# Performance work log

Measured on AMD Instinct MI355X. Metric: run time of the kernel, lower is better.

Reference implementation:

```python
import jax, jax.numpy as jnp
import numpy as np

NUM_TIME_BLOCKS = 32  # P
B, L, D = 32, 4096, 256


def setup_inputs() -> dict:
    key = jax.random.key(0)
    k1, k2 = jax.random.split(key)
    x = jax.random.normal(k1, (B, L, D), dtype=jnp.float32)
    # normalized timestamps in [0, 1), matching linspace(0, 1.001, P+1) bin edges
    time_steps = jax.random.uniform(k2, (B, L), dtype=jnp.float32)
    return {"x": x, "time_steps": time_steps}


def reference(x, time_steps):
    # Bin edges identical to torch.linspace(0.0, 1.001, P+1)
    blocks = jnp.linspace(0.0, 1.001, NUM_TIME_BLOCKS + 1, dtype=jnp.float32)
    ls = blocks[:-1]  # (P,) left edges (inclusive)
    rs = blocks[1:]   # (P,) right edges (exclusive)
    ts = time_steps[..., None]                      # (B, L, 1)
    # one-hot bucket membership mask, (B, L, P); a token falls in exactly one bin
    mask = ((ts >= ls) & (ts < rs)).astype(x.dtype)
    # sum x over sequence positions within each time bucket -> (B, P, D)
    new_x = jnp.einsum('blp,bld->bpd', mask, x)
    return new_x, time_steps
```

## Files before the change

### kernel.cpp

```cpp
#include <hip/hip_runtime.h>


#define Bk 32
#define Lk 4096
#define Dk 256
#define Pk 32

__device__ __forceinline__ int bucket_of(float tv) {
    const double step = 1.001 / 32.0;
    int p = (int)(tv * (float)(32.0 / 1.001));
    p = p < 0 ? 0 : (p > 31 ? 31 : p);
    while (p > 0 && tv < (float)((double)p * step)) --p;
    while (p < 31 && tv >= (float)((double)(p + 1) * step)) ++p;
    return p;
}

__global__ __launch_bounds__(256) void tc_fused(
        const float* __restrict__ x,
        const float* __restrict__ ts,
        float* __restrict__ out,
        float* __restrict__ ts_out) {
    __shared__ int rows[Lk];
    __shared__ int nrows;
    __shared__ float red[4 * Dk];

    const int p = blockIdx.x;
    const int b = blockIdx.y;
    const int t = threadIdx.x;
    const int w = t >> 6;
    const int lane = t & 63;
    const int col4 = lane << 2;

    if (t == 0) nrows = 0;
    __syncthreads();

    const float* tsb = ts + (size_t)b * Lk;
#pragma unroll
    for (int k = 0; k < Lk / 256; ++k) {
        const int l = t + k * 256;
        const float tv = tsb[l];
        if (p == 0) ts_out[(size_t)b * Lk + l] = tv;
        if (bucket_of(tv) == p) {
            const int idx = atomicAdd(&nrows, 1);
            rows[idx] = l;
        }
    }
    __syncthreads();
    const int cnt = nrows;

    const float* xb = x + (size_t)b * Lk * Dk;
    float4 a0 = make_float4(0.f, 0.f, 0.f, 0.f);
    float4 a1 = make_float4(0.f, 0.f, 0.f, 0.f);
    int i = w;
    for (; i + 4 < cnt; i += 8) {
        const int r0 = rows[i];
        const int r1 = rows[i + 4];
        const float4 v0 = *(const float4*)(xb + (size_t)r0 * Dk + col4);
        const float4 v1 = *(const float4*)(xb + (size_t)r1 * Dk + col4);
        a0.x += v0.x; a0.y += v0.y; a0.z += v0.z; a0.w += v0.w;
        a1.x += v1.x; a1.y += v1.y; a1.z += v1.z; a1.w += v1.w;
    }
    if (i < cnt) {
        const float4 v = *(const float4*)(xb + (size_t)rows[i] * Dk + col4);
        a0.x += v.x; a0.y += v.y; a0.z += v.z; a0.w += v.w;
    }
    a0.x += a1.x; a0.y += a1.y; a0.z += a1.z; a0.w += a1.w;

    *(float4*)&red[t * 4] = a0;
    __syncthreads();
    if (w == 0) {
        float4 r = *(float4*)&red[lane * 4];
#pragma unroll
        for (int ww = 1; ww < 4; ++ww) {
            const float4 o = *(const float4*)&red[(ww * 64 + lane) * 4];
            r.x += o.x; r.y += o.y; r.z += o.z; r.w += o.w;
        }
        *(float4*)(out + ((size_t)b * Pk + p) * Dk + col4) = r;
    }
}

extern "C" void kernel_launch(void* const* d_in, const int* in_sizes, int n_in,
                              void* d_out, int out_size, void* d_ws, size_t ws_size,
                              hipStream_t stream) {
    const float* x  = (const float*)d_in[0];
    const float* ts = (const float*)d_in[1];
    float* out = (float*)d_out;
    float* ts_out = out + (size_t)Bk * Pk * Dk;

    dim3 grid(Pk, Bk);
    tc_fused<<<grid, 256, 0, stream>>>(x, ts, out, ts_out);
}
```

Measured before the change: 203.6 us.

## Double block width, aggregate row compaction per wavefront, unroll gather by four

Raises the block size from 256 to 512 threads (8 wavefronts) and sets launch bounds to target higher occupancy. Row compaction now uses one ballot and popcount per wavefront with a single shared atomic, replacing one atomic per matching thread. The gather loop keeps four independent accumulators so more row loads are in flight. The cost is a larger cross-wavefront reduction and more register pressure.

```diff
diff --git a/kernel.cpp b/kernel.cpp
--- a/kernel.cpp
+++ b/kernel.cpp
@@ -5,6 +5,8 @@
 #define Lk 4096
 #define Dk 256
 #define Pk 32
+#define NT 512
+#define NW 8
 
 __device__ __forceinline__ int bucket_of(float tv) {
     const double step = 1.001 / 32.0;
@@ -15,14 +17,14 @@
     return p;
 }
 
-__global__ __launch_bounds__(256) void tc_fused(
+__global__ __launch_bounds__(NT, 8) void tc_fused(
         const float* __restrict__ x,
         const float* __restrict__ ts,
         float* __restrict__ out,
         float* __restrict__ ts_out) {
     __shared__ int rows[Lk];
     __shared__ int nrows;
-    __shared__ float red[4 * Dk];
+    __shared__ float red[NW * Dk];
 
     const int p = blockIdx.x;
     const int b = blockIdx.y;
@@ -36,13 +38,19 @@
 
     const float* tsb = ts + (size_t)b * Lk;
 #pragma unroll
-    for (int k = 0; k < Lk / 256; ++k) {
-        const int l = t + k * 256;
+    for (int k = 0; k < Lk / NT; ++k) {
+        const int l = t + k * NT;
         const float tv = tsb[l];
         if (p == 0) ts_out[(size_t)b * Lk + l] = tv;
-        if (bucket_of(tv) == p) {
-            const int idx = atomicAdd(&nrows, 1);
-            rows[idx] = l;
+        const bool match = (bucket_of(tv) == p);
+        const unsigned long long m = __ballot(match);
+        const int nact = __popcll(m);
+        int wbase = 0;
+        if (lane == 0 && nact) wbase = atomicAdd(&nrows, nact);
+        wbase = __shfl(wbase, 0);
+        if (match) {
+            const int pre = __popcll(m & ((1ull << lane) - 1ull));
+            rows[wbase + pre] = l;
         }
     }
     __syncthreads();
@@ -51,27 +59,37 @@
     const float* xb = x + (size_t)b * Lk * Dk;
     float4 a0 = make_float4(0.f, 0.f, 0.f, 0.f);
     float4 a1 = make_float4(0.f, 0.f, 0.f, 0.f);
+    float4 a2 = make_float4(0.f, 0.f, 0.f, 0.f);
+    float4 a3 = make_float4(0.f, 0.f, 0.f, 0.f);
     int i = w;
-    for (; i + 4 < cnt; i += 8) {
+    for (; i + 3 * NW < cnt; i += 4 * NW) {
         const int r0 = rows[i];
-        const int r1 = rows[i + 4];
+        const int r1 = rows[i + NW];
+        const int r2 = rows[i + 2 * NW];
+        const int r3 = rows[i + 3 * NW];
         const float4 v0 = *(const float4*)(xb + (size_t)r0 * Dk + col4);
         const float4 v1 = *(const float4*)(xb + (size_t)r1 * Dk + col4);
+        const float4 v2 = *(const float4*)(xb + (size_t)r2 * Dk + col4);
+        const float4 v3 = *(const float4*)(xb + (size_t)r3 * Dk + col4);
         a0.x += v0.x; a0.y += v0.y; a0.z += v0.z; a0.w += v0.w;
         a1.x += v1.x; a1.y += v1.y; a1.z += v1.z; a1.w += v1.w;
+        a2.x += v2.x; a2.y += v2.y; a2.z += v2.z; a2.w += v2.w;
+        a3.x += v3.x; a3.y += v3.y; a3.z += v3.z; a3.w += v3.w;
     }
-    if (i < cnt) {
+    for (; i < cnt; i += NW) {
         const float4 v = *(const float4*)(xb + (size_t)rows[i] * Dk + col4);
         a0.x += v.x; a0.y += v.y; a0.z += v.z; a0.w += v.w;
     }
     a0.x += a1.x; a0.y += a1.y; a0.z += a1.z; a0.w += a1.w;
+    a2.x += a3.x; a2.y += a3.y; a2.z += a3.z; a2.w += a3.w;
+    a0.x += a2.x; a0.y += a2.y; a0.z += a2.z; a0.w += a2.w;
 
     *(float4*)&red[t * 4] = a0;
     __syncthreads();
     if (w == 0) {
         float4 r = *(float4*)&red[lane * 4];
 #pragma unroll
-        for (int ww = 1; ww < 4; ++ww) {
+        for (int ww = 1; ww < NW; ++ww) {
             const float4 o = *(const float4*)&red[(ww * 64 + lane) * 4];
             r.x += o.x; r.y += o.y; r.z += o.z; r.w += o.w;
         }
@@ -88,5 +106,5 @@
     float* ts_out = out + (size_t)Bk * Pk * Dk;
 
     dim3 grid(Pk, Bk);
-    tc_fused<<<grid, 256, 0, stream>>>(x, ts, out, ts_out);
+    tc_fused<<<grid, NT, 0, stream>>>(x, ts, out, ts_out);
 }
```

Result: faster. 196.9 us (-3.3%).
